# Kernel optimization log

Hardware: AMD Instinct MI355X
Metric: run time of the kernel (lower is better)

Reference implementation:

```python
import jax, jax.numpy as jnp
import numpy as np

MUL = 8              # multiplicity of 0e and 1o irreps (feature dim = MUL + 3*MUL = 32)
N_NODES = 25000
N_EDGES = 200000
EDGE_ATTR_DIM = 16
RADIAL_HIDDEN = 64
N_PATHS = 5          # CG paths: 0e*0e->0e, 0e*1o->1o, 1o*0e->1o, 1o*1o->0e, 1o*1o->1o


def _split(x):
    # x: [*, MUL + 3*MUL] -> scalars [*, MUL], vectors [*, MUL, 3]
    return x[:, :MUL], x[:, MUL:].reshape(x.shape[0], MUL, 3)


def _radial(edge_attr, W1, W2):
    # two-layer radial net (e3nn FullyConnectedNet style, silu, fan-in normalized)
    h = jax.nn.silu(edge_attr @ W1 / jnp.sqrt(float(EDGE_ATTR_DIM)))
    w = h @ W2 / jnp.sqrt(float(RADIAL_HIDDEN))
    return w.reshape(-1, N_PATHS, MUL, MUL)  # [E, 5, MUL, MUL]


def _edge_tp(xs, xv, s0, s1, w):
    # per-edge FullyConnectedTensorProduct(irreps_in, irreps_sh, irreps_out)
    # xs:[E,MUL] xv:[E,MUL,3] s0:[E] s1:[E,3] w:[E,5,MUL,MUL]
    dot = jnp.einsum('emc,ec->em', xv, s1) / jnp.sqrt(3.0)          # 1o x 1o -> 0e
    out_s = (jnp.einsum('emn,em->en', w[:, 0], xs) * s0[:, None]
             + jnp.einsum('emn,em->en', w[:, 3], dot)) / jnp.sqrt(2.0 * MUL)
    cross = jnp.cross(xv, s1[:, None, :]) / jnp.sqrt(2.0)            # 1o x 1o -> 1o
    out_v = (jnp.einsum('emn,em->en', w[:, 1], xs)[:, :, None] * s1[:, None, :]
             + jnp.einsum('emn,emc->enc', w[:, 2], xv) * s0[:, None, None]
             + jnp.einsum('emn,emc->enc', w[:, 4], cross)) / jnp.sqrt(3.0 * MUL)
    return out_s, out_v


def setup_inputs() -> dict:
    key = jax.random.key(0)
    ks = jax.random.split(key, 12)
    node_attr = jax.random.normal(ks[0], (N_NODES, 4 * MUL), jnp.float32)
    edge_index = jax.random.randint(ks[1], (2, N_EDGES), 0, N_NODES, dtype=jnp.int32)
    edge_attr = jax.random.normal(ks[2], (N_EDGES, EDGE_ATTR_DIM), jnp.float32)
    edge_sh = jax.random.normal(ks[3], (N_EDGES, 4), jnp.float32)
    WSZ = N_PATHS * MUL * MUL
    return {
        'node_attr': node_attr,
        'edge_index': edge_index,
        'edge_attr': edge_attr,
        'edge_sh': edge_sh,
        'Wq0': jax.random.normal(ks[4], (MUL, MUL), jnp.float32),
        'Wq1': jax.random.normal(ks[5], (MUL, MUL), jnp.float32),
        'kW1': jax.random.normal(ks[6], (EDGE_ATTR_DIM, RADIAL_HIDDEN), jnp.float32),
        'kW2': jax.random.normal(ks[7], (RADIAL_HIDDEN, WSZ), jnp.float32),
        'vW1': jax.random.normal(ks[8], (EDGE_ATTR_DIM, RADIAL_HIDDEN), jnp.float32),
        'vW2': jax.random.normal(ks[9], (RADIAL_HIDDEN, WSZ), jnp.float32),
        'Wd0': jax.random.normal(ks[10], (MUL, MUL), jnp.float32),
        'Wd1': jax.random.normal(ks[11], (MUL, MUL), jnp.float32),
    }


def reference(node_attr, edge_index, edge_attr, edge_sh,
              Wq0, Wq1, kW1, kW2, vW1, vW2, Wd0, Wd1):
    src, dst = edge_index[0], edge_index[1]
    inv_sqrt_mul = 1.0 / jnp.sqrt(float(MUL))

    # q = o3.Linear(irreps_in -> irreps_query): mixes multiplicities within each irrep
    ns, nv = _split(node_attr)
    qs = ns @ Wq0 * inv_sqrt_mul                                   # [N, MUL]
    qv = jnp.einsum('nmc,mk->nkc', nv, Wq1) * inv_sqrt_mul          # [N, MUL, 3]

    # per-edge keys/values: gather src features, tensor product with edge_sh
    xs, xv = ns[src], nv[src]
    s0, s1 = edge_sh[:, 0], edge_sh[:, 1:4]
    wk = _radial(edge_attr, kW1, kW2)
    wv = _radial(edge_attr, vW1, vW2)
    ks_, kv_ = _edge_tp(xs, xv, s0, s1, wk)
    vs_, vv_ = _edge_tp(xs, xv, s0, s1, wv)

    # dot = FullyConnectedTensorProduct(query, key, '0e') per edge
    logits = (jnp.einsum('mn,em,en->e', Wd0, qs[dst], ks_)
              + jnp.einsum('mn,emc,enc->e', Wd1, qv[dst], kv_) / jnp.sqrt(3.0)
              ) / jnp.sqrt(2.0 * MUL)
    exp = jnp.exp(logits)[:, None]                                 # [E, 1]

    # scatter-mean normalization
    z_sum = jax.ops.segment_sum(exp, dst, num_segments=N_NODES)
    cnt = jax.ops.segment_sum(jnp.ones_like(exp), dst, num_segments=N_NODES)
    z = z_sum / jnp.maximum(cnt, 1.0)
    alpha = exp / z[dst]
    attn = jnp.sqrt(jax.nn.relu(alpha))

    # weighted scatter-sum aggregation
    v_edge = jnp.concatenate([vs_, vv_.reshape(-1, 3 * MUL)], axis=1)  # [E, 32]
    out = jax.ops.segment_sum(attn * v_edge, dst, num_segments=N_NODES)
    return out
```

## Files before the change

### kernel.cpp

```cpp
#include <hip/hip_runtime.h>
#include <hip/hip_bf16.h>
#include <math.h>

#define NE 200000
#define NN 25000

static constexpr float INV_SQRT3  = 0.5773502691896258f;
static constexpr float INV_SQRT2  = 0.7071067811865476f;
static constexpr float INV_SQRT8  = 0.3535533905932738f;
static constexpr float INV_SQRT24 = 0.2041241452319315f;

typedef __attribute__((ext_vector_type(8))) short bf16x8;
typedef __attribute__((ext_vector_type(4))) float f32x4;

union U16x8 { uint4 u; bf16x8 v; };

__device__ __forceinline__ unsigned f2bf1(float f) {
  unsigned u = __float_as_uint(f);
  return (u + 0x7FFFu + ((u >> 16) & 1u)) >> 16;
}
__device__ __forceinline__ unsigned packbf(float a, float b) {
  union { __hip_bfloat162 h; unsigned u; } c;
  c.h = __float22bfloat162_rn(make_float2(a, b));
  return c.u;
}
__device__ __forceinline__ float bflo(unsigned u) { return __uint_as_float(u << 16); }
__device__ __forceinline__ float bfhi(unsigned u) { return __uint_as_float(u & 0xFFFF0000u); }

__global__ __launch_bounds__(256) void prep_kernel(
    const float* __restrict__ kW1, const float* __restrict__ kW2,
    const float* __restrict__ vW1, const float* __restrict__ vW2,
    const float* __restrict__ node_attr,
    const float* __restrict__ Wq0, const float* __restrict__ Wq1,
    const float* __restrict__ Wd0, const float* __restrict__ Wd1,
    const int*   __restrict__ edge_index,
    unsigned short* __restrict__ afrag,
    unsigned short* __restrict__ afrag1,
    float* __restrict__ qd, float* __restrict__ qvd,
    int* __restrict__ hist)
{
  int t = blockIdx.x * blockDim.x + threadIdx.x;
  if (t < 4096) {
    int j    = t & 7;
    int lane = (t >> 3) & 63;
    int rt   = (t >> 9) & 3;
    int b    = (t >> 11) & 1;
    int quad = lane >> 4;
    int k    = quad * 8 + j;
    int jeff = k & 15;
    int r    = rt * 16 + (lane & 15);
    const float* W = b ? vW1 : kW1;
    afrag1[t] = (unsigned short)f2bf1(W[jeff * 64 + r]);
  }
  if (t < 40960) {
    int j    = t & 7;
    int lane = (t >> 3) & 63;
    int kk   = (t >> 9) & 1;
    int ot   = (t >> 10) & 1;
    int ci   = t >> 11;
    int b    = ci / 10;
    int rem  = ci - b * 10;
    int p    = rem >> 1;
    int hf   = rem & 1;
    int r    = kk * 32 + ((lane >> 4) << 3) + j;
    int o    = p * 64 + hf * 32 + ot * 16 + (lane & 15);
    const float* W = b ? vW2 : kW2;
    afrag[t] = (unsigned short)f2bf1(W[r * 320 + o]);
#pragma unroll
    for (int i = 0; i < 5; ++i) {
      int e = t * 5 + i;
      if (e < NE) atomicAdd(&hist[edge_index[NE + e]], 1);
    }
  }
  int tn = t - 40960;
  if (tn >= 0 && tn < NN) {
    int n = tn;
    float ns[8], nv[24];
#pragma unroll
    for (int i = 0; i < 8; ++i)  ns[i] = node_attr[n * 32 + i];
#pragma unroll
    for (int i = 0; i < 24; ++i) nv[i] = node_attr[n * 32 + 8 + i];
    float qs[8];
#pragma unroll
    for (int m = 0; m < 8; ++m) {
      float a = 0.f;
#pragma unroll
      for (int i = 0; i < 8; ++i) a = fmaf(ns[i], Wq0[i * 8 + m], a);
      qs[m] = a * INV_SQRT8;
    }
#pragma unroll
    for (int k = 0; k < 8; ++k) {
      float a = 0.f;
#pragma unroll
      for (int m = 0; m < 8; ++m) a = fmaf(qs[m], Wd0[m * 8 + k], a);
      qd[n * 8 + k] = a;
    }
    float qv[24];
#pragma unroll
    for (int k = 0; k < 8; ++k) {
#pragma unroll
      for (int c = 0; c < 3; ++c) {
        float a = 0.f;
#pragma unroll
        for (int m = 0; m < 8; ++m) a = fmaf(nv[m * 3 + c], Wq1[m * 8 + k], a);
        qv[k * 3 + c] = a * INV_SQRT8;
      }
    }
#pragma unroll
    for (int k = 0; k < 8; ++k) {
#pragma unroll
      for (int c = 0; c < 3; ++c) {
        float a = 0.f;
#pragma unroll
        for (int m = 0; m < 8; ++m) a = fmaf(qv[m * 3 + c], Wd1[m * 8 + k], a);
        qvd[n * 24 + k * 3 + c] = a;
      }
    }
  }
}

__global__ __launch_bounds__(1024) void scan_kernel(
    const int* __restrict__ hist, int* __restrict__ off, int* __restrict__ cursor)
{
  __shared__ int wsum[16];
  const int tid  = threadIdx.x;
  const int lane = tid & 63;
  const int wv   = tid >> 6;
  const int base = tid * 32;
  int loc[32];
  int s = 0;
  if (base < NN) {
    const int4* h4 = (const int4*)(hist + base);
#pragma unroll
    for (int q = 0; q < 8; ++q) {
      int4 v4 = h4[q];
      loc[4*q+0] = s; s += v4.x;
      loc[4*q+1] = s; s += v4.y;
      loc[4*q+2] = s; s += v4.z;
      loc[4*q+3] = s; s += v4.w;
    }
  } else {
#pragma unroll
    for (int i = 0; i < 32; ++i) loc[i] = 0;
  }
  int incl = s;
#pragma unroll
  for (int d = 1; d < 64; d <<= 1) {
    int t = __shfl_up(incl, d, 64);
    if (lane >= d) incl += t;
  }
  int wexcl = incl - s;
  if (lane == 63) wsum[wv] = incl;
  __syncthreads();
  if (wv == 0 && lane < 16) {
    int v = wsum[lane];
    int inc2 = v;
#pragma unroll
    for (int d = 1; d < 16; d <<= 1) {
      int t = __shfl_up(inc2, d, 64);
      if (lane >= d) inc2 += t;
    }
    wsum[lane] = inc2 - v;
  }
  __syncthreads();
  int tbase = wsum[wv] + wexcl;
  if (base < NN) {
#pragma unroll
    for (int i = 0; i < 32; ++i) {
      int idx = base + i;
      if (idx < NN) { int e2 = tbase + loc[i]; off[idx] = e2; cursor[idx] = e2; }
    }
  }
  if (tid == 1023) off[NN] = tbase + s;
}

__global__ __launch_bounds__(64) void edge_kernel(
    const float* __restrict__ node_attr,
    const int*   __restrict__ edge_index,
    const float* __restrict__ edge_attr,
    const float* __restrict__ edge_sh,
    const unsigned short* __restrict__ afrag1,
    const unsigned short* __restrict__ afrag,
    const float* __restrict__ qd,   const float* __restrict__ qvd,
    int* __restrict__ cursor,
    float* __restrict__ exo, float* __restrict__ wout)
{
  __shared__ unsigned char smem[9216];
  const int lane = threadIdx.x;
  const int l15  = lane & 15;
  const int quad = lane >> 4;
  unsigned char* sea = smem;
  unsigned char* sh  = smem;
  unsigned char* swp = smem;

  const int e = blockIdx.x * 64 + lane;
  const bool valid = (e < NE);
  const int el  = valid ? e : (NE - 1);
  const int src = edge_index[el];
  const int dst = edge_index[NE + el];

  int pos = 0;
  if (valid) pos = atomicAdd(&cursor[dst], 1);

  const float s0  = edge_sh[el * 4 + 0];
  const float s1x = edge_sh[el * 4 + 1];
  const float s1y = edge_sh[el * 4 + 2];
  const float s1z = edge_sh[el * 4 + 3];

  {
    float ea[16];
    const float4* ea4 = (const float4*)(edge_attr + (size_t)el * 16);
#pragma unroll
    for (int i = 0; i < 4; ++i) {
      float4 v = ea4[i];
      ea[4*i+0] = v.x; ea[4*i+1] = v.y; ea[4*i+2] = v.z; ea[4*i+3] = v.w;
    }
    unsigned char* myrow = sea + lane * 80;
    unsigned hi[8];
    float lo[16];
#pragma unroll
    for (int i = 0; i < 8; ++i) {
      unsigned pk = packbf(ea[2*i], ea[2*i+1]);
      hi[i] = pk;
      lo[2*i]   = ea[2*i]   - bflo(pk);
      lo[2*i+1] = ea[2*i+1] - bfhi(pk);
    }
    uint4 w0 = {hi[0], hi[1], hi[2], hi[3]};
    uint4 w1 = {hi[4], hi[5], hi[6], hi[7]};
    *(uint4*)(myrow)      = w0;
    *(uint4*)(myrow + 16) = w1;
    uint4 w2, w3;
    w2.x = packbf(lo[0], lo[1]);   w2.y = packbf(lo[2], lo[3]);
    w2.z = packbf(lo[4], lo[5]);   w2.w = packbf(lo[6], lo[7]);
    w3.x = packbf(lo[8], lo[9]);   w3.y = packbf(lo[10], lo[11]);
    w3.z = packbf(lo[12], lo[13]); w3.w = packbf(lo[14], lo[15]);
    *(uint4*)(myrow + 32) = w2;
    *(uint4*)(myrow + 48) = w3;
  }

  U16x8 B1[4];
#pragma unroll
  for (int et = 0; et < 4; ++et)
    B1[et].u = *(const uint4*)(sea + (et*16 + l15) * 80 + quad * 16);

  float xs[8], xv[8][3];
  {
    const float4* na4 = (const float4*)(node_attr + (size_t)src * 32);
    float tmp[32];
#pragma unroll
    for (int i = 0; i < 8; ++i) {
      float4 v = na4[i];
      tmp[4*i+0] = v.x; tmp[4*i+1] = v.y; tmp[4*i+2] = v.z; tmp[4*i+3] = v.w;
    }
#pragma unroll
    for (int m = 0; m < 8; ++m) xs[m] = tmp[m];
#pragma unroll
    for (int m = 0; m < 8; ++m) {
      xv[m][0] = tmp[8 + 3*m + 0];
      xv[m][1] = tmp[8 + 3*m + 1];
      xv[m][2] = tmp[8 + 3*m + 2];
    }
  }

  const uint4* AF  = (const uint4*)afrag;
  const uint4* AF1 = (const uint4*)afrag1;
  float ex = 0.f;

#pragma unroll 1
  for (int b = 0; b < 2; ++b) {
    U16x8 a00, a01, a10, a11;
    {
      const int ci = b * 10;
      a00.u = AF[(ci*4 + 0) * 64 + lane];
      a01.u = AF[(ci*4 + 1) * 64 + lane];
      a10.u = AF[(ci*4 + 2) * 64 + lane];
      a11.u = AF[(ci*4 + 3) * 64 + lane];
    }

    U16x8 a1;
    a1.u = AF1[(b * 4 + 0) * 64 + lane];
#pragma unroll 1
    for (int rt = 0; rt < 4; ++rt) {
      f32x4 c[4];
#pragma unroll
      for (int et = 0; et < 4; ++et) {
        f32x4 cz = {0.f, 0.f, 0.f, 0.f};
        c[et] = __builtin_amdgcn_mfma_f32_16x16x32_bf16(a1.v, B1[et].v, cz, 0, 0, 0);
      }
      if (rt < 3) a1.u = AF1[(b * 4 + rt + 1) * 64 + lane];
#pragma unroll
      for (int et = 0; et < 4; ++et) {
        float hh[4];
#pragma unroll
        for (int i = 0; i < 4; ++i) {
          float x = c[et][i] * 0.25f;
          hh[i] = x / (1.f + __expf(-x));
        }
        uint2 pk;
        pk.x = packbf(hh[0], hh[1]);
        pk.y = packbf(hh[2], hh[3]);
        *(uint2*)(sh + (et*16 + l15) * 144 + (rt*16 + quad*4) * 2) = pk;
      }
    }

    bf16x8 B[4][2];
#pragma unroll
    for (int et = 0; et < 4; ++et) {
#pragma unroll
      for (int kk = 0; kk < 2; ++kk) {
        U16x8 cv;
        cv.u = *(const uint4*)(sh + (et*16 + l15) * 144 + kk * 64 + quad * 16);
        B[et][kk] = cv.v;
      }
    }

    float accs[8];
    float accv[8][3];
#pragma unroll
    for (int n = 0; n < 8; ++n) {
      accs[n] = 0.f;
      accv[n][0] = 0.f; accv[n][1] = 0.f; accv[n][2] = 0.f;
    }

#pragma unroll 1
    for (int cc = 0; cc < 10; ++cc) {
      const int p  = cc >> 1;
      const int hf = cc & 1;

#pragma unroll
      for (int et = 0; et < 4; ++et) {
        f32x4 c0 = {0.f, 0.f, 0.f, 0.f};
        f32x4 c1 = {0.f, 0.f, 0.f, 0.f};
        c0 = __builtin_amdgcn_mfma_f32_16x16x32_bf16(a00.v, B[et][0], c0, 0, 0, 0);
        c0 = __builtin_amdgcn_mfma_f32_16x16x32_bf16(a01.v, B[et][1], c0, 0, 0, 0);
        c1 = __builtin_amdgcn_mfma_f32_16x16x32_bf16(a10.v, B[et][0], c1, 0, 0, 0);
        c1 = __builtin_amdgcn_mfma_f32_16x16x32_bf16(a11.v, B[et][1], c1, 0, 0, 0);
        unsigned char* wrow = swp + (et*16 + l15) * 144;
        *(f32x4*)(wrow + quad * 16)      = c0;
        *(f32x4*)(wrow + 64 + quad * 16) = c1;
      }

      const float4* wr = (const float4*)(swp + (size_t)lane * 144);
      float4 qa = wr[0], qb = wr[1], qc = wr[2], qd2 = wr[3];
      if (cc < 9) {
        const int cn = b * 10 + cc + 1;
        a00.u = AF[(cn*4 + 0) * 64 + lane];
        a01.u = AF[(cn*4 + 1) * 64 + lane];
        a10.u = AF[(cn*4 + 2) * 64 + lane];
        a11.u = AF[(cn*4 + 3) * 64 + lane];
      }

#pragma unroll
      for (int h2 = 0; h2 < 2; ++h2) {
        float4 ra, rb, rc, rd;
        if (h2 == 0) { ra = qa; rb = qb; rc = qc; rd = qd2; }
        else         { ra = wr[4]; rb = wr[5]; rc = wr[6]; rd = wr[7]; }
        float wvv[16] = {ra.x,ra.y,ra.z,ra.w, rb.x,rb.y,rb.z,rb.w,
                         rc.x,rc.y,rc.z,rc.w, rd.x,rd.y,rd.z,rd.w};
#pragma unroll
        for (int mm = 0; mm < 2; ++mm) {
          const int m = hf * 4 + h2 * 2 + mm;
          const float* wm = &wvv[mm * 8];
          if (p == 0) {
            float g = xs[m] * s0;
#pragma unroll
            for (int n = 0; n < 8; ++n) accs[n] = fmaf(wm[n], g, accs[n]);
          } else if (p == 1) {
            float a = xs[m];
            float gx = a * s1x, gy = a * s1y, gz = a * s1z;
#pragma unroll
            for (int n = 0; n < 8; ++n) {
              accv[n][0] = fmaf(wm[n], gx, accv[n][0]);
              accv[n][1] = fmaf(wm[n], gy, accv[n][1]);
              accv[n][2] = fmaf(wm[n], gz, accv[n][2]);
            }
          } else if (p == 2) {
            float gx = xv[m][0] * s0, gy = xv[m][1] * s0, gz = xv[m][2] * s0;
#pragma unroll
            for (int n = 0; n < 8; ++n) {
              accv[n][0] = fmaf(wm[n], gx, accv[n][0]);
              accv[n][1] = fmaf(wm[n], gy, accv[n][1]);
              accv[n][2] = fmaf(wm[n], gz, accv[n][2]);
            }
          } else if (p == 3) {
            float dm = (xv[m][0]*s1x + xv[m][1]*s1y + xv[m][2]*s1z) * INV_SQRT3;
#pragma unroll
            for (int n = 0; n < 8; ++n) accs[n] = fmaf(wm[n], dm, accs[n]);
          } else {
            float crx = (xv[m][1]*s1z - xv[m][2]*s1y) * INV_SQRT2;
            float cry = (xv[m][2]*s1x - xv[m][0]*s1z) * INV_SQRT2;
            float crz = (xv[m][0]*s1y - xv[m][1]*s1x) * INV_SQRT2;
#pragma unroll
            for (int n = 0; n < 8; ++n) {
              accv[n][0] = fmaf(wm[n], crx, accv[n][0]);
              accv[n][1] = fmaf(wm[n], cry, accv[n][1]);
              accv[n][2] = fmaf(wm[n], crz, accv[n][2]);
            }
          }
        }
      }
    }

    if (b == 0) {
      float lg = 0.f, lv = 0.f;
#pragma unroll
      for (int n = 0; n < 8; ++n) lg = fmaf(accs[n], qd[dst * 8 + n], lg);
#pragma unroll
      for (int n = 0; n < 8; ++n) {
#pragma unroll
        for (int c = 0; c < 3; ++c)
          lv = fmaf(accv[n][c], qvd[dst * 24 + n * 3 + c], lv);
      }
      float logit = (lg * (1.f / 32.f) +
                     lv * (0.125f * INV_SQRT24) * INV_SQRT3) * 0.25f;
      ex = __expf(logit);
      if (valid) exo[pos] = ex;
    } else {
      if (valid) {
        float a = sqrtf(ex);
        const float ss = a * (1.f / 32.f);
        const float sv = a * (0.125f * INV_SQRT24);
        float4* v4 = (float4*)(wout + (size_t)pos * 32);
        float4 o;
        o.x = accs[0] * ss; o.y = accs[1] * ss;
        o.z = accs[2] * ss; o.w = accs[3] * ss;
        v4[0] = o;
        o.x = accs[4] * ss; o.y = accs[5] * ss;
        o.z = accs[6] * ss; o.w = accs[7] * ss;
        v4[1] = o;
        o.x = accv[0][0] * sv; o.y = accv[0][1] * sv;
        o.z = accv[0][2] * sv; o.w = accv[1][0] * sv;
        v4[2] = o;
        o.x = accv[1][1] * sv; o.y = accv[1][2] * sv;
        o.z = accv[2][0] * sv; o.w = accv[2][1] * sv;
        v4[3] = o;
        o.x = accv[2][2] * sv; o.y = accv[3][0] * sv;
        o.z = accv[3][1] * sv; o.w = accv[3][2] * sv;
        v4[4] = o;
        o.x = accv[4][0] * sv; o.y = accv[4][1] * sv;
        o.z = accv[4][2] * sv; o.w = accv[5][0] * sv;
        v4[5] = o;
        o.x = accv[5][1] * sv; o.y = accv[5][2] * sv;
        o.z = accv[6][0] * sv; o.w = accv[6][1] * sv;
        v4[6] = o;
        o.x = accv[6][2] * sv; o.y = accv[7][0] * sv;
        o.z = accv[7][1] * sv; o.w = accv[7][2] * sv;
        v4[7] = o;
      }
    }
  }
}

__global__ __launch_bounds__(256) void gather_kernel(
    const int* __restrict__ off,
    const float* __restrict__ exo,
    const float* __restrict__ wout,
    float* __restrict__ out)
{
  const int tid  = threadIdx.x;
  const int wave = tid >> 6;
  const int lane = tid & 63;
  const int n = blockIdx.x * 4 + wave;
  if (n >= NN) return;
  const int start = off[n];
  const int end   = off[n + 1];
  const int cnt   = end - start;

  float zp = 0.f;
  for (int j = start + lane; j < end; j += 64) zp += exo[j];
#pragma unroll
  for (int s = 32; s >= 1; s >>= 1) zp += __shfl_xor(zp, s, 64);

  const int q  = lane & 7;
  const int rr = lane >> 3;
  float4 acc = {0.f, 0.f, 0.f, 0.f};
  const float4* w4 = (const float4*)wout;
  for (int j = start + rr; j < end; j += 8) {
    float4 v = w4[(size_t)j * 8 + q];
    acc.x += v.x; acc.y += v.y; acc.z += v.z; acc.w += v.w;
  }
#pragma unroll
  for (int s = 8; s < 64; s <<= 1) {
    acc.x += __shfl_xor(acc.x, s, 64);
    acc.y += __shfl_xor(acc.y, s, 64);
    acc.z += __shfl_xor(acc.z, s, 64);
    acc.w += __shfl_xor(acc.w, s, 64);
  }
  if (rr == 0) {
    float s = (cnt > 0 && zp > 0.f) ? sqrtf((float)cnt / zp) : 0.f;
    float4 o = {acc.x * s, acc.y * s, acc.z * s, acc.w * s};
    ((float4*)out)[(size_t)n * 8 + q] = o;
  }
}

extern "C" void kernel_launch(void* const* d_in, const int* in_sizes, int n_in,
                              void* d_out, int out_size, void* d_ws, size_t ws_size,
                              hipStream_t stream)
{
  const float* node_attr  = (const float*)d_in[0];
  const int*   edge_index = (const int*)  d_in[1];
  const float* edge_attr  = (const float*)d_in[2];
  const float* edge_sh    = (const float*)d_in[3];
  const float* Wq0 = (const float*)d_in[4];
  const float* Wq1 = (const float*)d_in[5];
  const float* kW1 = (const float*)d_in[6];
  const float* kW2 = (const float*)d_in[7];
  const float* vW1 = (const float*)d_in[8];
  const float* vW2 = (const float*)d_in[9];
  const float* Wd0 = (const float*)d_in[10];
  const float* Wd1 = (const float*)d_in[11];
  float* out = (float*)d_out;

  float* ws = (float*)d_ws;
  float* qd     = ws;
  float* qvd    = qd   + 200000;
  unsigned short* afrag  = (unsigned short*)(qvd + 600000);
  unsigned short* afrag1 = afrag + 40960;
  int* hist   = (int*)(afrag1 + 4096);
  int* off    = hist + 25024;
  int* cursor = off  + 25056;
  float* exo  = (float*)(cursor + 25024);
  float* wout = exo + 200000;

  hipMemsetAsync(hist, 0, 25024 * sizeof(int), stream);

  prep_kernel<<<259, 256, 0, stream>>>(
      kW1, kW2, vW1, vW2, node_attr, Wq0, Wq1, Wd0, Wd1, edge_index,
      afrag, afrag1, qd, qvd, hist);
  scan_kernel<<<1, 1024, 0, stream>>>(hist, off, cursor);
  edge_kernel<<<(NE + 63) / 64, 64, 0, stream>>>(
      node_attr, edge_index, edge_attr, edge_sh,
      afrag1, afrag, qd, qvd, cursor, exo, wout);
  gather_kernel<<<(NN + 3) / 4, 256, 0, stream>>>(off, exo, wout, out);
}
```

Baseline: 209.6 us.

## Fuse prefix scan into prep kernel via last-block pattern; batch gather nodes per wave

After: 272.8 us. +30.2%, slower.

```diff
diff --git a/kernel.cpp b/kernel.cpp
--- a/kernel.cpp
+++ b/kernel.cpp
@@ -37,7 +37,8 @@
     unsigned short* __restrict__ afrag,
     unsigned short* __restrict__ afrag1,
     float* __restrict__ qd, float* __restrict__ qvd,
-    int* __restrict__ hist)
+    int* __restrict__ hist, int* __restrict__ done,
+    int* __restrict__ off,  int* __restrict__ cursor)
 {
   int t = blockIdx.x * blockDim.x + threadIdx.x;
   if (t < 4096) {
@@ -117,61 +118,50 @@
       }
     }
   }
-}
-
-__global__ __launch_bounds__(1024) void scan_kernel(
-    const int* __restrict__ hist, int* __restrict__ off, int* __restrict__ cursor)
-{
-  __shared__ int wsum[16];
+
+  __threadfence();
+  __shared__ int amLast;
+  if (threadIdx.x == 0) {
+    int prev = atomicAdd(done, 1);
+    amLast = (prev == (int)gridDim.x - 1) ? 1 : 0;
+  }
+  __syncthreads();
+  if (!amLast) return;
+
   const int tid  = threadIdx.x;
   const int lane = tid & 63;
   const int wv   = tid >> 6;
-  const int base = tid * 32;
-  int loc[32];
+  const int base = tid * 98;
   int s = 0;
-  if (base < NN) {
-    const int4* h4 = (const int4*)(hist + base);
-#pragma unroll
-    for (int q = 0; q < 8; ++q) {
-      int4 v4 = h4[q];
-      loc[4*q+0] = s; s += v4.x;
-      loc[4*q+1] = s; s += v4.y;
-      loc[4*q+2] = s; s += v4.z;
-      loc[4*q+3] = s; s += v4.w;
-    }
-  } else {
-#pragma unroll
-    for (int i = 0; i < 32; ++i) loc[i] = 0;
+  for (int i = 0; i < 98; ++i) {
+    int idx = base + i;
+    if (idx < NN) s += hist[idx];
   }
   int incl = s;
 #pragma unroll
   for (int d = 1; d < 64; d <<= 1) {
-    int t = __shfl_up(incl, d, 64);
-    if (lane >= d) incl += t;
-  }
-  int wexcl = incl - s;
-  if (lane == 63) wsum[wv] = incl;
+    int t2 = __shfl_up(incl, d, 64);
+    if (lane >= d) incl += t2;
+  }
+  __shared__ int wsum2[4];
+  __shared__ int wbase[4];
+  if (lane == 63) wsum2[wv] = incl;
   __syncthreads();
-  if (wv == 0 && lane < 16) {
-    int v = wsum[lane];
-    int inc2 = v;
-#pragma unroll
-    for (int d = 1; d < 16; d <<= 1) {
-      int t = __shfl_up(inc2, d, 64);
-      if (lane >= d) inc2 += t;
-    }
-    wsum[lane] = inc2 - v;
+  if (tid == 0) {
+    int acc = 0;
+#pragma unroll
+    for (int w = 0; w < 4; ++w) { wbase[w] = acc; acc += wsum2[w]; }
+    off[NN] = acc;
   }
   __syncthreads();
-  int tbase = wsum[wv] + wexcl;
-  if (base < NN) {
-#pragma unroll
-    for (int i = 0; i < 32; ++i) {
-      int idx = base + i;
-      if (idx < NN) { int e2 = tbase + loc[i]; off[idx] = e2; cursor[idx] = e2; }
-    }
-  }
-  if (tid == 1023) off[NN] = tbase + s;
+  int running = wbase[wv] + (incl - s);
+  for (int i = 0; i < 98; ++i) {
+    int idx = base + i;
+    if (idx < NN) {
+      off[idx] = running; cursor[idx] = running;
+      running += hist[idx];
+    }
+  }
 }
 
 __global__ __launch_bounds__(64) void edge_kernel(
@@ -460,36 +450,41 @@
   const int tid  = threadIdx.x;
   const int wave = tid >> 6;
   const int lane = tid & 63;
-  const int n = blockIdx.x * 4 + wave;
-  if (n >= NN) return;
-  const int start = off[n];
-  const int end   = off[n + 1];
-  const int cnt   = end - start;
-
-  float zp = 0.f;
-  for (int j = start + lane; j < end; j += 64) zp += exo[j];
-#pragma unroll
-  for (int s = 32; s >= 1; s >>= 1) zp += __shfl_xor(zp, s, 64);
-
-  const int q  = lane & 7;
-  const int rr = lane >> 3;
-  float4 acc = {0.f, 0.f, 0.f, 0.f};
-  const float4* w4 = (const float4*)wout;
-  for (int j = start + rr; j < end; j += 8) {
-    float4 v = w4[(size_t)j * 8 + q];
-    acc.x += v.x; acc.y += v.y; acc.z += v.z; acc.w += v.w;
-  }
-#pragma unroll
-  for (int s = 8; s < 64; s <<= 1) {
-    acc.x += __shfl_xor(acc.x, s, 64);
-    acc.y += __shfl_xor(acc.y, s, 64);
-    acc.z += __shfl_xor(acc.z, s, 64);
-    acc.w += __shfl_xor(acc.w, s, 64);
-  }
-  if (rr == 0) {
-    float s = (cnt > 0 && zp > 0.f) ? sqrtf((float)cnt / zp) : 0.f;
-    float4 o = {acc.x * s, acc.y * s, acc.z * s, acc.w * s};
-    ((float4*)out)[(size_t)n * 8 + q] = o;
+  const int nbase = blockIdx.x * 16 + wave * 4;
+
+#pragma unroll 1
+  for (int k = 0; k < 4; ++k) {
+    const int n = nbase + k;
+    if (n >= NN) return;
+    const int start = off[n];
+    const int end   = off[n + 1];
+    const int cnt   = end - start;
+
+    float zp = 0.f;
+    for (int j = start + lane; j < end; j += 64) zp += exo[j];
+#pragma unroll
+    for (int s = 32; s >= 1; s >>= 1) zp += __shfl_xor(zp, s, 64);
+
+    const int q  = lane & 7;
+    const int rr = lane >> 3;
+    float4 acc = {0.f, 0.f, 0.f, 0.f};
+    const float4* w4 = (const float4*)wout;
+    for (int j = start + rr; j < end; j += 8) {
+      float4 v = w4[(size_t)j * 8 + q];
+      acc.x += v.x; acc.y += v.y; acc.z += v.z; acc.w += v.w;
+    }
+#pragma unroll
+    for (int s = 8; s < 64; s <<= 1) {
+      acc.x += __shfl_xor(acc.x, s, 64);
+      acc.y += __shfl_xor(acc.y, s, 64);
+      acc.z += __shfl_xor(acc.z, s, 64);
+      acc.w += __shfl_xor(acc.w, s, 64);
+    }
+    if (rr == 0) {
+      float s = (cnt > 0 && zp > 0.f) ? sqrtf((float)cnt / zp) : 0.f;
+      float4 o = {acc.x * s, acc.y * s, acc.z * s, acc.w * s};
+      ((float4*)out)[(size_t)n * 8 + q] = o;
+    }
   }
 }
 
@@ -517,19 +512,19 @@
   unsigned short* afrag  = (unsigned short*)(qvd + 600000);
   unsigned short* afrag1 = afrag + 40960;
   int* hist   = (int*)(afrag1 + 4096);
-  int* off    = hist + 25024;
+  int* done   = hist + 25024;
+  int* off    = done + 16;
   int* cursor = off  + 25056;
   float* exo  = (float*)(cursor + 25024);
   float* wout = exo + 200000;
 
-  hipMemsetAsync(hist, 0, 25024 * sizeof(int), stream);
+  hipMemsetAsync(hist, 0, (25024 + 16) * sizeof(int), stream);
 
   prep_kernel<<<259, 256, 0, stream>>>(
       kW1, kW2, vW1, vW2, node_attr, Wq0, Wq1, Wd0, Wd1, edge_index,
-      afrag, afrag1, qd, qvd, hist);
-  scan_kernel<<<1, 1024, 0, stream>>>(hist, off, cursor);
+      afrag, afrag1, qd, qvd, hist, done, off, cursor);
   edge_kernel<<<(NE + 63) / 64, 64, 0, stream>>>(
       node_attr, edge_index, edge_attr, edge_sh,
       afrag1, afrag, qd, qvd, cursor, exo, wout);
-  gather_kernel<<<(NN + 3) / 4, 256, 0, stream>>>(off, exo, wout, out);
+  gather_kernel<<<(NN + 15) / 16, 256, 0, stream>>>(off, exo, wout, out);
 }
```
